# Optimization experiments

Hardware: AMD Instinct MI355X
Metric: run time of the kernel (lower is better)

Reference implementation:

```python
import jax, jax.numpy as jnp
import numpy as np

P, B, L = 32, 64, 128
E, HB, HP = 64, 128, 128   # byte emb dim, byte GRU hidden, packet GRU hidden
PE = 2 * HB                # packet embedding dim = 256
LH = 128                   # attention linear hidden
NC = 10                    # num classes


def _gru_dir(x, w_ih, w_hh, b_ih, b_hh, reverse=False):
    # x: [T, N, E_in] -> outputs [T, N, H]; PyTorch GRU gate math, h0 = 0.
    H = w_hh.shape[1]
    xg = jnp.einsum('tne,ge->tng', x, w_ih) + b_ih  # precompute input gates [T,N,3H]
    if reverse:
        xg = xg[::-1]

    def step(h, xgt):
        hg = h @ w_hh.T + b_hh
        xr, xz, xn = jnp.split(xgt, 3, axis=-1)
        hr, hz, hn = jnp.split(hg, 3, axis=-1)
        r = jax.nn.sigmoid(xr + hr)
        z = jax.nn.sigmoid(xz + hz)
        n = jnp.tanh(xn + r * hn)
        h = (1.0 - z) * n + z * h
        return h, h

    h0 = jnp.zeros((x.shape[1], H), x.dtype)
    _, ys = jax.lax.scan(step, h0, xg)
    if reverse:
        ys = ys[::-1]
    return ys


def _bigru(x, wif, whf, bif, bhf, wib, whb, bib, bhb):
    f = _gru_dir(x, wif, whf, bif, bhf, reverse=False)
    b = _gru_dir(x, wib, whb, bib, bhb, reverse=True)
    return jnp.concatenate([f, b], axis=-1)


def setup_inputs() -> dict:
    key = jax.random.key(0)
    ks = jax.random.split(key, 32)
    rn = lambda k, shp: (jax.random.normal(k, shp, dtype=jnp.float32) * 0.05)
    inp = {}
    inp['flow'] = jax.random.randint(ks[0], (P, B, L), 0, 256, dtype=jnp.int64)
    inp['emb'] = rn(ks[1], (256, E))
    # byte biGRU (forward / backward dirs)
    inp['byte_wih_f'] = rn(ks[2], (3 * HB, E)); inp['byte_whh_f'] = rn(ks[3], (3 * HB, HB))
    inp['byte_bih_f'] = rn(ks[4], (3 * HB,));   inp['byte_bhh_f'] = rn(ks[5], (3 * HB,))
    inp['byte_wih_b'] = rn(ks[6], (3 * HB, E)); inp['byte_whh_b'] = rn(ks[7], (3 * HB, HB))
    inp['byte_bih_b'] = rn(ks[8], (3 * HB,));   inp['byte_bhh_b'] = rn(ks[9], (3 * HB,))
    # packet biGRU
    inp['pkt_wih_f'] = rn(ks[10], (3 * HP, PE)); inp['pkt_whh_f'] = rn(ks[11], (3 * HP, HP))
    inp['pkt_bih_f'] = rn(ks[12], (3 * HP,));    inp['pkt_bhh_f'] = rn(ks[13], (3 * HP,))
    inp['pkt_wih_b'] = rn(ks[14], (3 * HP, PE)); inp['pkt_whh_b'] = rn(ks[15], (3 * HP, HP))
    inp['pkt_bih_b'] = rn(ks[16], (3 * HP,));    inp['pkt_bhh_b'] = rn(ks[17], (3 * HP,))
    # byte attention (Linear(2HB->LH), Linear(LH->1))
    inp['ba_w1'] = rn(ks[18], (LH, 2 * HB)); inp['ba_b1'] = rn(ks[19], (LH,))
    inp['ba_w2'] = rn(ks[20], (1, LH));      inp['ba_b2'] = rn(ks[21], (1,))
    # packet attention (Linear(2HP->LH), Linear(LH->1))
    inp['pa_w1'] = rn(ks[22], (LH, 2 * HP)); inp['pa_b1'] = rn(ks[23], (LH,))
    inp['pa_w2'] = rn(ks[24], (1, LH));      inp['pa_b2'] = rn(ks[25], (1,))
    # final classifier
    inp['wf'] = rn(ks[26], (NC, 2 * HP)); inp['bf'] = rn(ks[27], (NC,))
    return inp


def reference(flow, emb,
              byte_wih_f, byte_whh_f, byte_bih_f, byte_bhh_f,
              byte_wih_b, byte_whh_b, byte_bih_b, byte_bhh_b,
              pkt_wih_f, pkt_whh_f, pkt_bih_f, pkt_bhh_f,
              pkt_wih_b, pkt_whh_b, pkt_bih_b, pkt_bhh_b,
              ba_w1, ba_b1, ba_w2, ba_b2,
              pa_w1, pa_b1, pa_w2, pa_b2,
              wf, bf):
    p, b, l = flow.shape
    x = emb[flow]                                   # [P,B,L,E]
    # batch the per-packet byte GRU across packets: [L, P*B, E]
    xb = x.transpose(2, 0, 1, 3).reshape(l, p * b, E)
    out = _bigru(xb, byte_wih_f, byte_whh_f, byte_bih_f, byte_bhh_f,
                 byte_wih_b, byte_whh_b, byte_bih_b, byte_bhh_b)  # [L, P*B, 2HB]
    out = out.reshape(l, p, b, 2 * HB)
    # Attention: tanh(lin1) -> lin2 -> softmax over dim=1 of the [L,B,1] view,
    # i.e. over the batch axis (faithful to the original code).
    h = jnp.tanh(jnp.einsum('lpbd,hd->lpbh', out, ba_w1) + ba_b1)
    score = jnp.einsum('lpbh,oh->lpbo', h, ba_w2) + ba_b2          # [L,P,B,1]
    attn = jax.nn.softmax(score, axis=2)
    packet_emb = (out * attn).sum(axis=0)                          # [P,B,2HB]
    # packet biGRU over packet sequence
    out2 = _bigru(packet_emb, pkt_wih_f, pkt_whh_f, pkt_bih_f, pkt_bhh_f,
                  pkt_wih_b, pkt_whh_b, pkt_bih_b, pkt_bhh_b)      # [P,B,2HP]
    h2 = jnp.tanh(jnp.einsum('pbd,hd->pbh', out2, pa_w1) + pa_b1)
    score2 = jnp.einsum('pbh,oh->pbo', h2, pa_w2) + pa_b2          # [P,B,1]
    attn2 = jax.nn.softmax(score2, axis=1)
    flow_emb = (out2 * attn2).sum(axis=1)                          # [P,2HP] (faithful sum over dim=1)
    return flow_emb @ wf.T + bf                                    # [P,NC]
```

## Files before the change

kernel.cpp:

```cpp
#include <hip/hip_runtime.h>
#include <hip/hip_bf16.h>
#include <hip/hip_fp16.h>
#include <cstdint>
#include <cstddef>


#define DINLINE __device__ __forceinline__

typedef _Float16 f16;
typedef f16 f16x8 __attribute__((ext_vector_type(8)));
typedef float f32x4 __attribute__((ext_vector_type(4)));

static DINLINE float fast_sigmoid(float x) {
    const float e = __builtin_amdgcn_exp2f(-1.44269504089f * x);
    return __builtin_amdgcn_rcpf(1.0f + e);
}
static DINLINE float fast_tanh(float x) {
    const float e = __builtin_amdgcn_exp2f(2.88539008178f * x);
    return 1.0f - 2.0f * __builtin_amdgcn_rcpf(1.0f + e);
}

static DINLINE void lds_barrier() {
    asm volatile("s_waitcnt lgkmcnt(0)\n\ts_barrier" ::: "memory");
    __builtin_amdgcn_sched_barrier(0);
}

__global__ void k_tables(const float* __restrict__ emb,
                         const float* __restrict__ wihF, const float* __restrict__ bihF,
                         const float* __restrict__ bhhF,
                         const float* __restrict__ wihB, const float* __restrict__ bihB,
                         const float* __restrict__ bhhB,
                         float4* __restrict__ tab4F, float4* __restrict__ tab4B) {
    const int v = blockIdx.x & 255;
    const int dir = blockIdx.x >> 8;
    const float* wih = dir ? wihB : wihF;
    const float* bih = dir ? bihB : bihF;
    const float* bhh = dir ? bhhB : bhhF;
    float4* tab4 = dir ? tab4B : tab4F;
    __shared__ float er[64];
    __shared__ float sh[384];
    if (threadIdx.x < 64) er[threadIdx.x] = emb[v * 64 + threadIdx.x];
    __syncthreads();
    const int g = threadIdx.x;
    float acc = bih[g] + (g < 256 ? bhh[g] : 0.0f);
    #pragma unroll
    for (int e = 0; e < 64; ++e) acc = fmaf(wih[g * 64 + e], er[e], acc);
    sh[g] = acc;
    __syncthreads();
    if (g < 128) {
        float4 pk;
        pk.x = sh[g];
        pk.y = sh[g + 128];
        pk.z = sh[g + 256];
        pk.w = 0.f;
        tab4[v * 128 + g] = pk;
    }
}

struct TransArgs {
    const float* src[2];
    float* dst[2];
    int R[2];
    int C[2];
};
__global__ void k_transpose(TransArgs a) {
    const int m = blockIdx.y;
    const float* __restrict__ s = a.src[m];
    float* __restrict__ d = a.dst[m];
    const int R = a.R[m], C = a.C[m];
    const int total = R * C;
    for (int idx = blockIdx.x * blockDim.x + threadIdx.x; idx < total;
         idx += gridDim.x * blockDim.x) {
        const int r = idx / C, c = idx - r * C;
        d[c * R + r] = s[idx];
    }
}

__global__ __launch_bounds__(512, 1) void k_byte_gru(
    const int* __restrict__ flow,
    const float4* __restrict__ tab4F, const float4* __restrict__ tab4B,
    const float* __restrict__ whhF, const float* __restrict__ whhB,
    const float* __restrict__ bhhF, const float* __restrict__ bhhB,
    __half* __restrict__ hF, __half* __restrict__ hB) {
    const int dir = blockIdx.x & 1;
    const int chunk = blockIdx.x >> 1;
    const int row0 = chunk * 16;
    const int tid = threadIdx.x;
    const int wid = tid >> 6;
    const int lane = tid & 63;
    const int c = lane & 15;
    const int q = lane >> 4;
    const int j = wid * 16 + c;

    const float4* __restrict__ t4 = dir ? tab4B : tab4F;
    const float* __restrict__ whh = dir ? whhB : whhF;
    const float* __restrict__ bhh = dir ? bhhB : bhhF;
    __half* __restrict__ hout = dir ? hB : hF;

    __shared__ f16 hbuf[2][16 * 128];
    __shared__ int flow_lds[16][128];

    for (int i = tid; i < 16 * 128; i += 512)
        flow_lds[i >> 7][i & 127] = flow[row0 * 128 + i] & 255;
    for (int i = tid; i < 16 * 128; i += 512) hbuf[0][i] = (f16)0.f;

    f16x8 Bf[3][4];
    #pragma unroll
    for (int g = 0; g < 3; ++g) {
        #pragma unroll
        for (int ks = 0; ks < 4; ++ks) {
            const float* src = whh + (size_t)(g * 128 + j) * 128 + ks * 32 + q * 8;
            f16x8 b;
            #pragma unroll
            for (int e = 0; e < 8; ++e) b[e] = (f16)src[e];
            Bf[g][ks] = b;
        }
    }
    const float bh2 = bhh[j + 256];
    float hold[4];
    #pragma unroll
    for (int rr = 0; rr < 4; ++rr) hold[rr] = 0.f;
    __syncthreads();

    for (int t = 0; t < 128; ++t) {
        const int curb = t & 1, nxtb = curb ^ 1;
        const int tt = dir ? (127 - t) : t;

        float4 x4[4];
        #pragma unroll
        for (int rr = 0; rr < 4; ++rr)
            x4[rr] = t4[flow_lds[q * 4 + rr][tt] * 128 + j];

        f16x8 Af[4];
        #pragma unroll
        for (int ks = 0; ks < 4; ++ks) {
            const int kb = ks * 32 + q * 8;
            const int idx = c * 128 + (kb ^ ((c & 7) << 3));
            Af[ks] = *reinterpret_cast<const f16x8*>(&hbuf[curb][idx]);
        }

        f32x4 a0 = {0.f, 0.f, 0.f, 0.f};
        f32x4 a1 = {0.f, 0.f, 0.f, 0.f};
        f32x4 a2 = {0.f, 0.f, 0.f, 0.f};
        #pragma unroll
        for (int ks = 0; ks < 4; ++ks) {
            a0 = __builtin_amdgcn_mfma_f32_16x16x32_f16(Af[ks], Bf[0][ks], a0, 0, 0, 0);
            a1 = __builtin_amdgcn_mfma_f32_16x16x32_f16(Af[ks], Bf[1][ks], a1, 0, 0, 0);
            a2 = __builtin_amdgcn_mfma_f32_16x16x32_f16(Af[ks], Bf[2][ks], a2, 0, 0, 0);
        }

        #pragma unroll
        for (int rr = 0; rr < 4; ++rr) {
            const float rg = fast_sigmoid(x4[rr].x + a0[rr]);
            const float zg = fast_sigmoid(x4[rr].y + a1[rr]);
            const float ng = fast_tanh(x4[rr].z + rg * (a2[rr] + bh2));
            const float hn = fmaf(zg, hold[rr] - ng, ng);
            hold[rr] = hn;
            const int row = q * 4 + rr;
            hbuf[nxtb][row * 128 + (j ^ ((row & 7) << 3))] = (f16)hn;
        }
        lds_barrier();

        {
            const int row = tid >> 5;
            const int ho = (tid & 31) * 4;
            const int idx = row * 128 + (ho ^ ((row & 7) << 3));
            const uint2 v = *reinterpret_cast<const uint2*>(&hbuf[nxtb][idx]);
            *reinterpret_cast<uint2*>(
                &hout[((size_t)tt * 2048 + row0 + row) * 128 + ho]) = v;
        }
    }
}

__global__ __launch_bounds__(256, 1) void k_scores_attn(
    const __half* __restrict__ hF, const __half* __restrict__ hB,
    const float* __restrict__ w1,
    const float* __restrict__ b1, const float* __restrict__ w2,
    const float* __restrict__ b2, float* __restrict__ attn) {
    __shared__ f16 w1lds[128 * 256];
    __shared__ float sc[128];
    const int tid = threadIdx.x;
    for (int i = tid; i < 128 * 256; i += 256) {
        const int col = i >> 8, k = i & 255;
        w1lds[col * 256 + (k ^ ((col & 7) << 3))] = (f16)w1[i];
    }
    const int lane = tid & 63, w = tid >> 6;
    const int c = lane & 15, q = lane >> 4;

    float b1v[8], w2v[8];
    #pragma unroll
    for (int ct = 0; ct < 8; ++ct) {
        b1v[ct] = b1[ct * 16 + c];
        w2v[ct] = w2[ct * 16 + c];
    }
    const float b2v = b2[0];
    __syncthreads();

    for (int it = 0; it < 4; ++it) {
        const int pos0 = blockIdx.x * 512 + it * 128;

        f16x8 Af[2][8];
        #pragma unroll
        for (int pt = 0; pt < 2; ++pt) {
            const size_t pos = (size_t)pos0 + (w * 2 + pt) * 16 + c;
            const f16* hFp = (const f16*)(hF + pos * 128);
            const f16* hBp = (const f16*)(hB + pos * 128);
            #pragma unroll
            for (int ks = 0; ks < 4; ++ks)
                Af[pt][ks] = *reinterpret_cast<const f16x8*>(hFp + ks * 32 + q * 8);
            #pragma unroll
            for (int ks = 0; ks < 4; ++ks)
                Af[pt][4 + ks] = *reinterpret_cast<const f16x8*>(hBp + ks * 32 + q * 8);
        }

        float s[2][4] = {{0.f, 0.f, 0.f, 0.f}, {0.f, 0.f, 0.f, 0.f}};
        #pragma unroll
        for (int ct = 0; ct < 8; ++ct) {
            const int jj = ct * 16 + c;
            f16x8 Bfr[8];
            #pragma unroll
            for (int ks = 0; ks < 8; ++ks) {
                const int k = ks * 32 + q * 8;
                Bfr[ks] = *reinterpret_cast<const f16x8*>(
                    &w1lds[jj * 256 + (k ^ ((jj & 7) << 3))]);
            }
            #pragma unroll
            for (int pt = 0; pt < 2; ++pt) {
                f32x4 acc = {0.f, 0.f, 0.f, 0.f};
                #pragma unroll
                for (int ks = 0; ks < 8; ++ks)
                    acc = __builtin_amdgcn_mfma_f32_16x16x32_f16(Af[pt][ks],
                                                                 Bfr[ks], acc,
                                                                 0, 0, 0);
                #pragma unroll
                for (int rr = 0; rr < 4; ++rr)
                    s[pt][rr] += w2v[ct] * fast_tanh(acc[rr] + b1v[ct]);
            }
        }
        #pragma unroll
        for (int pt = 0; pt < 2; ++pt) {
            #pragma unroll
            for (int rr = 0; rr < 4; ++rr) {
                float v = s[pt][rr];
                v += __shfl_xor(v, 1);
                v += __shfl_xor(v, 2);
                v += __shfl_xor(v, 4);
                v += __shfl_xor(v, 8);
                if (c == 0) sc[(w * 2 + pt) * 16 + q * 4 + rr] = v + b2v;
            }
        }
        __syncthreads();
        if (tid < 128) {
            const float sv = sc[tid];
            float m = sv;
            for (int off = 32; off; off >>= 1) m = fmaxf(m, __shfl_xor(m, off));
            const float e = __expf(sv - m);
            float sum = e;
            for (int off = 32; off; off >>= 1) sum += __shfl_xor(sum, off);
            attn[pos0 + tid] = e / sum;
        }
        __syncthreads();
    }
}

__global__ __launch_bounds__(256) void k_packet_emb(
    const __half* __restrict__ hF, const __half* __restrict__ hB,
    const float* __restrict__ attn, float* __restrict__ pe) {
    const int tid = threadIdx.x;
    const int g = tid >> 6;
    const int lane = tid & 63;
    const int n = blockIdx.x * 4 + g;
    const bool isF = lane < 32;
    const int chunk = lane & 31;
    const __half* __restrict__ hsrc = (isF ? hF : hB) + (size_t)n * 128 + chunk * 4;
    float acc0 = 0.f, acc1 = 0.f, acc2 = 0.f, acc3 = 0.f;
    #pragma unroll 4
    for (int l = 0; l < 128; ++l) {
        const float wv = attn[l * 2048 + n];
        const uint2 u = *reinterpret_cast<const uint2*>(hsrc + (size_t)l * 2048 * 128);
        const f16* hv = reinterpret_cast<const f16*>(&u);
        acc0 = fmaf(wv, (float)hv[0], acc0);
        acc1 = fmaf(wv, (float)hv[1], acc1);
        acc2 = fmaf(wv, (float)hv[2], acc2);
        acc3 = fmaf(wv, (float)hv[3], acc3);
    }
    float4 o = {acc0, acc1, acc2, acc3};
    *reinterpret_cast<float4*>(&pe[n * 256 + (isF ? 0 : 128) + chunk * 4]) = o;
}

__global__ __launch_bounds__(384) void k_pkt_xg(
    const float* __restrict__ pe, const float* __restrict__ wihTF,
    const float* __restrict__ bihF, const float* __restrict__ bhhF,
    const float* __restrict__ wihTB, const float* __restrict__ bihB,
    const float* __restrict__ bhhB, float4* __restrict__ xg4F,
    float4* __restrict__ xg4B) {
    const int dir = blockIdx.y;
    const float* __restrict__ wihT = dir ? wihTB : wihTF;
    const float* __restrict__ bih = dir ? bihB : bihF;
    const float* __restrict__ bhh = dir ? bhhB : bhhF;
    float4* __restrict__ xg4 = dir ? xg4B : xg4F;
    const int rbase = blockIdx.x * 8;
    __shared__ float xrow[8][256];
    __shared__ float sh[8][384];
    for (int i = threadIdx.x; i < 8 * 256; i += 384)
        xrow[i >> 8][i & 255] = pe[rbase * 256 + i];
    __syncthreads();
    const int g = threadIdx.x;
    float acc[8];
    const float bias = bih[g] + (g < 256 ? bhh[g] : 0.0f);
    #pragma unroll
    for (int r = 0; r < 8; ++r) acc[r] = bias;
    for (int d = 0; d < 256; ++d) {
        const float w = wihT[d * 384 + g];
        #pragma unroll
        for (int r = 0; r < 8; ++r) acc[r] = fmaf(w, xrow[r][d], acc[r]);
    }
    #pragma unroll
    for (int r = 0; r < 8; ++r) sh[r][g] = acc[r];
    __syncthreads();
    for (int i = threadIdx.x; i < 8 * 128; i += 384) {
        const int r = i >> 7, jj = i & 127;
        float4 pk;
        pk.x = sh[r][jj];
        pk.y = sh[r][jj + 128];
        pk.z = sh[r][jj + 256];
        pk.w = 0.f;
        xg4[(size_t)(rbase + r) * 128 + jj] = pk;
    }
}

__global__ __launch_bounds__(512, 1) void k_pkt_gru(
    const float4* __restrict__ xg4F, const float4* __restrict__ xg4B,
    const float* __restrict__ whhF, const float* __restrict__ whhB,
    const float* __restrict__ bhhF, const float* __restrict__ bhhB,
    float* __restrict__ h2F, float* __restrict__ h2B) {
    const int dir = blockIdx.x & 1;
    const int chunk = blockIdx.x >> 1;
    const int row0 = chunk * 16;
    const int tid = threadIdx.x;
    const int wid = tid >> 6;
    const int lane = tid & 63;
    const int c = lane & 15;
    const int q = lane >> 4;
    const int j = wid * 16 + c;

    const float4* __restrict__ xg4 = dir ? xg4B : xg4F;
    const float* __restrict__ whh = dir ? whhB : whhF;
    const float* __restrict__ bhh = dir ? bhhB : bhhF;
    float* __restrict__ hout = dir ? h2B : h2F;

    __shared__ f16 hbuf[2][16 * 128];

    for (int i = tid; i < 16 * 128; i += 512) hbuf[0][i] = (f16)0.f;

    f16x8 Bf[3][4];
    #pragma unroll
    for (int g = 0; g < 3; ++g) {
        #pragma unroll
        for (int ks = 0; ks < 4; ++ks) {
            const float* src = whh + (size_t)(g * 128 + j) * 128 + ks * 32 + q * 8;
            f16x8 b;
            #pragma unroll
            for (int e = 0; e < 8; ++e) b[e] = (f16)src[e];
            Bf[g][ks] = b;
        }
    }
    const float bh2 = bhh[j + 256];
    float hold[4];
    #pragma unroll
    for (int rr = 0; rr < 4; ++rr) hold[rr] = 0.f;
    __syncthreads();

    for (int t = 0; t < 32; ++t) {
        const int curb = t & 1, nxtb = curb ^ 1;
        const int tt = dir ? (31 - t) : t;

        float4 x4[4];
        #pragma unroll
        for (int rr = 0; rr < 4; ++rr)
            x4[rr] = xg4[(size_t)(tt * 64 + row0 + q * 4 + rr) * 128 + j];

        f16x8 Af[4];
        #pragma unroll
        for (int ks = 0; ks < 4; ++ks) {
            const int kb = ks * 32 + q * 8;
            const int idx = c * 128 + (kb ^ ((c & 7) << 3));
            Af[ks] = *reinterpret_cast<const f16x8*>(&hbuf[curb][idx]);
        }

        f32x4 a0 = {0.f, 0.f, 0.f, 0.f};
        f32x4 a1 = {0.f, 0.f, 0.f, 0.f};
        f32x4 a2 = {0.f, 0.f, 0.f, 0.f};
        #pragma unroll
        for (int ks = 0; ks < 4; ++ks) {
            a0 = __builtin_amdgcn_mfma_f32_16x16x32_f16(Af[ks], Bf[0][ks], a0, 0, 0, 0);
            a1 = __builtin_amdgcn_mfma_f32_16x16x32_f16(Af[ks], Bf[1][ks], a1, 0, 0, 0);
            a2 = __builtin_amdgcn_mfma_f32_16x16x32_f16(Af[ks], Bf[2][ks], a2, 0, 0, 0);
        }

        #pragma unroll
        for (int rr = 0; rr < 4; ++rr) {
            const float rg = fast_sigmoid(x4[rr].x + a0[rr]);
            const float zg = fast_sigmoid(x4[rr].y + a1[rr]);
            const float ng = fast_tanh(x4[rr].z + rg * (a2[rr] + bh2));
            const float hn = fmaf(zg, hold[rr] - ng, ng);
            hold[rr] = hn;
            const int row = q * 4 + rr;
            hbuf[nxtb][row * 128 + (j ^ ((row & 7) << 3))] = (f16)hn;
            hout[((size_t)tt * 64 + row0 + row) * 128 + j] = hn;
        }
        lds_barrier();
    }
}

__global__ __launch_bounds__(128) void k_scores2(
    const float* __restrict__ h2F, const float* __restrict__ h2B,
    const float* __restrict__ paw1,
    const float* __restrict__ pab1, const float* __restrict__ paw2,
    const float* __restrict__ pab2, float* __restrict__ scores2) {
    const int n = blockIdx.x;
    const int tid = threadIdx.x;
    __shared__ float x[256];
    __shared__ float red[2];
    x[tid] = h2F[n * 128 + tid];
    x[tid + 128] = h2B[n * 128 + tid];
    __syncthreads();
    float acc = pab1[tid];
    const float* wr = paw1 + tid * 256;
    #pragma unroll 8
    for (int d = 0; d < 256; ++d) acc = fmaf(wr[d], x[d], acc);
    float s = paw2[tid] * fast_tanh(acc);
    s += __shfl_xor(s, 1);
    s += __shfl_xor(s, 2);
    s += __shfl_xor(s, 4);
    s += __shfl_xor(s, 8);
    s += __shfl_xor(s, 16);
    s += __shfl_xor(s, 32);
    if ((tid & 63) == 0) red[tid >> 6] = s;
    __syncthreads();
    if (tid == 0) scores2[n] = red[0] + red[1] + pab2[0];
}

__global__ __launch_bounds__(256) void k_final3(
    const float* __restrict__ h2F, const float* __restrict__ h2B,
    const float* __restrict__ scores2, const float* __restrict__ wf,
    const float* __restrict__ bfv, float* __restrict__ outp) {
    const int p = blockIdx.x;
    const int tid = threadIdx.x;
    __shared__ float sc[64];
    __shared__ float femb[256];
    __shared__ float red[64];

    if (tid < 64) {
        const float s = scores2[p * 64 + tid];
        float m = s;
        for (int off = 32; off; off >>= 1) m = fmaxf(m, __shfl_xor(m, off));
        const float e = __expf(s - m);
        float sum = e;
        for (int off = 32; off; off >>= 1) sum += __shfl_xor(sum, off);
        sc[tid] = e / sum;
    }
    __syncthreads();

    {
        const float* __restrict__ hsrc = (tid < 128) ? h2F : h2B;
        const int d = tid & 127;
        float acc = 0.f;
        for (int b = 0; b < 64; ++b)
            acc = fmaf(sc[b], hsrc[(p * 64 + b) * 128 + d], acc);
        femb[tid] = acc;
    }
    __syncthreads();

    const float fv = femb[tid];
    #pragma unroll
    for (int c = 0; c < 10; ++c) {
        float s = fv * wf[c * 256 + tid];
        s += __shfl_xor(s, 1);
        s += __shfl_xor(s, 2);
        s += __shfl_xor(s, 4);
        s += __shfl_xor(s, 8);
        s += __shfl_xor(s, 16);
        s += __shfl_xor(s, 32);
        if ((tid & 63) == 0) red[(c << 2) | (tid >> 6)] = s;
        __syncthreads();
        if (tid == 0)
            outp[p * 10 + c] = bfv[c] + red[c << 2] + red[(c << 2) | 1] +
                               red[(c << 2) | 2] + red[(c << 2) | 3];
        __syncthreads();
    }
}

extern "C" void kernel_launch(void* const* d_in, const int* in_sizes, int n_in,
                              void* d_out, int out_size, void* d_ws,
                              size_t ws_size, hipStream_t stream) {
    const int* flow = (const int*)d_in[0];
    const float* emb = (const float*)d_in[1];
    const float* byte_wih_f = (const float*)d_in[2];
    const float* byte_whh_f = (const float*)d_in[3];
    const float* byte_bih_f = (const float*)d_in[4];
    const float* byte_bhh_f = (const float*)d_in[5];
    const float* byte_wih_b = (const float*)d_in[6];
    const float* byte_whh_b = (const float*)d_in[7];
    const float* byte_bih_b = (const float*)d_in[8];
    const float* byte_bhh_b = (const float*)d_in[9];
    const float* pkt_wih_f = (const float*)d_in[10];
    const float* pkt_whh_f = (const float*)d_in[11];
    const float* pkt_bih_f = (const float*)d_in[12];
    const float* pkt_bhh_f = (const float*)d_in[13];
    const float* pkt_wih_b = (const float*)d_in[14];
    const float* pkt_whh_b = (const float*)d_in[15];
    const float* pkt_bih_b = (const float*)d_in[16];
    const float* pkt_bhh_b = (const float*)d_in[17];
    const float* ba_w1 = (const float*)d_in[18];
    const float* ba_b1 = (const float*)d_in[19];
    const float* ba_w2 = (const float*)d_in[20];
    const float* ba_b2 = (const float*)d_in[21];
    const float* pa_w1 = (const float*)d_in[22];
    const float* pa_b1 = (const float*)d_in[23];
    const float* pa_w2 = (const float*)d_in[24];
    const float* pa_b2 = (const float*)d_in[25];
    const float* wf = (const float*)d_in[26];
    const float* bf = (const float*)d_in[27];

    char* base = (char*)d_ws;
    size_t off = 0;
    auto allocf = [&](size_t nf) -> float* {
        float* p = (float*)(base + off);
        off += nf * sizeof(float);
        return p;
    };
    auto alloch = [&](size_t nh) -> __half* {
        off = (off + 255) & ~(size_t)255;
        __half* p = (__half*)(base + off);
        off += nh * sizeof(__half);
        return p;
    };
    float* wihTpF = allocf(256 * 384);
    float* wihTpB = allocf(256 * 384);
    float* attn = allocf(262144);
    float* pe = allocf(2048 * 256);
    float4* tab4F = (float4*)allocf(256 * 128 * 4);
    float4* tab4B = (float4*)allocf(256 * 128 * 4);
    float4* xg4F = (float4*)allocf((size_t)2048 * 128 * 4);
    float4* xg4B = (float4*)allocf((size_t)2048 * 128 * 4);
    float* h2F = allocf(32 * 64 * 128);
    float* h2B = allocf(32 * 64 * 128);
    float* scores2 = allocf(2048);
    __half* hF = alloch((size_t)128 * 2048 * 128);
    __half* hB = alloch((size_t)128 * 2048 * 128);
    if (off > ws_size) return;
    (void)in_sizes; (void)n_in; (void)out_size;

    k_tables<<<512, 384, 0, stream>>>(emb, byte_wih_f, byte_bih_f, byte_bhh_f,
                                      byte_wih_b, byte_bih_b, byte_bhh_b,
                                      tab4F, tab4B);

    TransArgs ta;
    ta.src[0] = pkt_wih_f; ta.dst[0] = wihTpF; ta.R[0] = 384; ta.C[0] = 256;
    ta.src[1] = pkt_wih_b; ta.dst[1] = wihTpB; ta.R[1] = 384; ta.C[1] = 256;
    k_transpose<<<dim3(96, 2), 256, 0, stream>>>(ta);

    k_byte_gru<<<256, 512, 0, stream>>>(flow, tab4F, tab4B, byte_whh_f,
                                        byte_whh_b, byte_bhh_f, byte_bhh_b, hF,
                                        hB);

    k_scores_attn<<<512, 256, 0, stream>>>(hF, hB, ba_w1, ba_b1, ba_w2, ba_b2,
                                           attn);
    k_packet_emb<<<512, 256, 0, stream>>>(hF, hB, attn, pe);

    k_pkt_xg<<<dim3(256, 2), 384, 0, stream>>>(pe, wihTpF, pkt_bih_f,
                                               pkt_bhh_f, wihTpB, pkt_bih_b,
                                               pkt_bhh_b, xg4F, xg4B);
    k_pkt_gru<<<8, 512, 0, stream>>>(xg4F, xg4B, pkt_whh_f, pkt_whh_b,
                                     pkt_bhh_f, pkt_bhh_b, h2F, h2B);
    k_scores2<<<2048, 128, 0, stream>>>(h2F, h2B, pa_w1, pa_b1, pa_w2, pa_b2,
                                        scores2);
    k_final3<<<32, 256, 0, stream>>>(h2F, h2B, scores2, wf, bf, (float*)d_out);
}
```

Measured before the change: 288.4 us.

## Halve rows per byte-GRU block to double grid and use all CUs

The byte GRU kernel now processes 8 sequence rows per block instead of 16, doubling the grid from 256 to 512 blocks so that all compute units on the device get work. Only 2 of the 4 MFMA output rows per lane quad are real, so half of each 16x16 MFMA tile is wasted padding. Launch bounds are raised to allow multiple blocks per CU. The flow indices are prescaled into byte offsets so the table gather needs less address arithmetic.

After: 303.4 us. 5.2% more time.

```diff
diff --git a/kernel.cpp b/kernel.cpp
--- a/kernel.cpp
+++ b/kernel.cpp
@@ -76,7 +76,7 @@
     }
 }
 
-__global__ __launch_bounds__(512, 1) void k_byte_gru(
+__global__ __launch_bounds__(512, 4) void k_byte_gru(
     const int* __restrict__ flow,
     const float4* __restrict__ tab4F, const float4* __restrict__ tab4B,
     const float* __restrict__ whhF, const float* __restrict__ whhB,
@@ -84,7 +84,7 @@
     __half* __restrict__ hF, __half* __restrict__ hB) {
     const int dir = blockIdx.x & 1;
     const int chunk = blockIdx.x >> 1;
-    const int row0 = chunk * 16;
+    const int row0 = chunk * 8;
     const int tid = threadIdx.x;
     const int wid = tid >> 6;
     const int lane = tid & 63;
@@ -92,17 +92,21 @@
     const int q = lane >> 4;
     const int j = wid * 16 + c;
 
-    const float4* __restrict__ t4 = dir ? tab4B : tab4F;
+    const char* __restrict__ t4 =
+        reinterpret_cast<const char*>(dir ? tab4B : tab4F);
     const float* __restrict__ whh = dir ? whhB : whhF;
     const float* __restrict__ bhh = dir ? bhhB : bhhF;
     __half* __restrict__ hout = dir ? hB : hF;
 
     __shared__ f16 hbuf[2][16 * 128];
-    __shared__ int flow_lds[16][128];
-
-    for (int i = tid; i < 16 * 128; i += 512)
-        flow_lds[i >> 7][i & 127] = flow[row0 * 128 + i] & 255;
-    for (int i = tid; i < 16 * 128; i += 512) hbuf[0][i] = (f16)0.f;
+    __shared__ int flow_lds[8][128];
+
+    for (int i = tid; i < 8 * 128; i += 512)
+        flow_lds[i >> 7][i & 127] = (flow[row0 * 128 + i] & 255) << 11;
+    {
+        f16* hb = reinterpret_cast<f16*>(hbuf);
+        for (int i = tid; i < 2 * 16 * 128; i += 512) hb[i] = (f16)0.f;
+    }
 
     f16x8 Bf[3][4];
     #pragma unroll
@@ -117,19 +121,18 @@
         }
     }
     const float bh2 = bhh[j + 256];
-    float hold[4];
-    #pragma unroll
-    for (int rr = 0; rr < 4; ++rr) hold[rr] = 0.f;
+    float hold[2] = {0.f, 0.f};
     __syncthreads();
 
     for (int t = 0; t < 128; ++t) {
         const int curb = t & 1, nxtb = curb ^ 1;
         const int tt = dir ? (127 - t) : t;
 
-        float4 x4[4];
-        #pragma unroll
-        for (int rr = 0; rr < 4; ++rr)
-            x4[rr] = t4[flow_lds[q * 4 + rr][tt] * 128 + j];
+        float4 x4[2];
+        #pragma unroll
+        for (int rr = 0; rr < 2; ++rr)
+            x4[rr] = *reinterpret_cast<const float4*>(
+                t4 + flow_lds[q * 2 + rr][tt] + (j << 4));
 
         f16x8 Af[4];
         #pragma unroll
@@ -150,24 +153,25 @@
         }
 
         #pragma unroll
-        for (int rr = 0; rr < 4; ++rr) {
+        for (int rr = 0; rr < 2; ++rr) {
             const float rg = fast_sigmoid(x4[rr].x + a0[rr]);
             const float zg = fast_sigmoid(x4[rr].y + a1[rr]);
             const float ng = fast_tanh(x4[rr].z + rg * (a2[rr] + bh2));
             const float hn = fmaf(zg, hold[rr] - ng, ng);
             hold[rr] = hn;
-            const int row = q * 4 + rr;
-            hbuf[nxtb][row * 128 + (j ^ ((row & 7) << 3))] = (f16)hn;
+            const int slot = q * 4 + rr;
+            hbuf[nxtb][slot * 128 + (j ^ ((slot & 7) << 3))] = (f16)hn;
         }
         lds_barrier();
 
         {
-            const int row = tid >> 5;
-            const int ho = (tid & 31) * 4;
-            const int idx = row * 128 + (ho ^ ((row & 7) << 3));
-            const uint2 v = *reinterpret_cast<const uint2*>(&hbuf[nxtb][idx]);
-            *reinterpret_cast<uint2*>(
-                &hout[((size_t)tt * 2048 + row0 + row) * 128 + ho]) = v;
+            const int pr = wid;
+            const int slot = ((pr >> 1) << 2) | (pr & 1);
+            const int ho = lane * 2;
+            const int idx = slot * 128 + (ho ^ ((slot & 7) << 3));
+            const uint32_t v = *reinterpret_cast<const uint32_t*>(&hbuf[nxtb][idx]);
+            *reinterpret_cast<uint32_t*>(
+                &hout[((size_t)tt * 2048 + row0 + pr) * 128 + ho]) = v;
         }
     }
 }
@@ -561,7 +565,7 @@
     ta.src[1] = pkt_wih_b; ta.dst[1] = wihTpB; ta.R[1] = 384; ta.C[1] = 256;
     k_transpose<<<dim3(96, 2), 256, 0, stream>>>(ta);
 
-    k_byte_gru<<<256, 512, 0, stream>>>(flow, tab4F, tab4B, byte_whh_f,
+    k_byte_gru<<<512, 512, 0, stream>>>(flow, tab4F, tab4B, byte_whh_f,
                                         byte_whh_b, byte_bhh_f, byte_bhh_b, hF,
                                         hB);
 
```
